# Optimization experiments

Measured on AMD Instinct MI355X. Metric: run time of the kernel, lower is better.

The kernel has to match this reference:

```python
import jax, jax.numpy as jnp
import numpy as np

B, T, D_IN, H, D_MU, K = 512, 256, 64, 256, 32, 8
EPS = 1e-09
ALPHA = 1.0


def setup_inputs() -> dict:
    key = jax.random.key(0)
    ks = jax.random.split(key, 32)
    def n(k, shape, s=0.05):
        return (jax.random.normal(k, shape) * s).astype(jnp.float32)
    X = jax.random.normal(ks[0], (B, T, D_IN), dtype=jnp.float32)
    missing_mask = (jax.random.uniform(ks[1], (B, T, D_IN)) < 0.8).astype(jnp.float32)
    noise = jax.random.normal(ks[2], (B, D_MU), dtype=jnp.float32)
    return dict(
        X=X, missing_mask=missing_mask, noise=noise,
        W_imp=n(ks[3], (D_IN, D_IN)),
        enc_Wih=n(ks[4], (4 * H, D_IN)), enc_bih=n(ks[5], (4 * H,)),
        enc_Whh=n(ks[6], (4 * H, H)), enc_bhh=n(ks[7], (4 * H,)),
        enc_Wch=n(ks[8], (3 * H, H)), enc_bch=n(ks[9], (3 * H,)),
        dec_Wih=n(ks[10], (4 * H, D_IN)), dec_bih=n(ks[11], (4 * H,)),
        dec_Whh=n(ks[12], (4 * H, H)), dec_bhh=n(ks[13], (4 * H,)),
        dec_Wch=n(ks[14], (3 * H, H)), dec_bch=n(ks[15], (3 * H,)),
        ae_enc_W=n(ks[16], (H, H)), ae_enc_b=n(ks[17], (H,)),
        ae_dec_W=n(ks[18], (H, D_MU)), ae_dec_b=n(ks[19], (H,)),
        mu_W=n(ks[20], (D_MU, H)), mu_b=n(ks[21], (D_MU,)),
        std_W=n(ks[22], (D_MU, H)), std_b=n(ks[23], (D_MU,)),
        out_W=n(ks[24], (D_IN, H)), out_b=n(ks[25], (D_IN,)),
        mu_c_u=n(ks[26], (K, D_MU)), var_c_u=n(ks[27], (K, D_MU)),
        phi_c_u=n(ks[28], (K,)),
    )


def _peephole_scan(xs, h0, c0, Wih, bih, Whh, bhh, Wch, bch):
    # xs: [T, B, D]; peephole LSTM with 3H-wide cell->gate weights (i, f, o),
    # gate layout of the 4H preactivation is (i, f, g, o) with g getting no peephole.
    Hd = h0.shape[1]
    def step(carry, x):
        h, c = carry
        wx = x @ Wih.T + bih          # [B, 4H]
        wh = h @ Whh.T + bhh          # [B, 4H]
        wc = c @ Wch.T + bch          # [B, 3H]
        wc_full = jnp.concatenate(
            [wc[:, :2 * Hd], jnp.zeros_like(h), wc[:, 2 * Hd:]], axis=1)
        s = wx + wh + wc_full
        i = jax.nn.sigmoid(s[:, :Hd])
        f = jax.nn.sigmoid(s[:, Hd:2 * Hd])
        g = jnp.tanh(s[:, 2 * Hd:3 * Hd])
        o = jax.nn.sigmoid(s[:, 3 * Hd:])
        c_new = f * c + i * g
        h_new = o * jnp.tanh(c_new)
        return (h_new, c_new), h_new
    (h, c), hs = jax.lax.scan(step, (h0, c0), xs)
    return h, c, hs


def reference(X, missing_mask, noise, W_imp,
              enc_Wih, enc_bih, enc_Whh, enc_bhh, enc_Wch, enc_bch,
              dec_Wih, dec_bih, dec_Whh, dec_bhh, dec_Wch, dec_bch,
              ae_enc_W, ae_enc_b, ae_dec_W, ae_dec_b,
              mu_W, mu_b, std_W, std_b, out_W, out_b,
              mu_c_u, var_c_u, phi_c_u):
    b, t, d_in = X.shape
    # --- implicit imputation (faithful to original, incl. (1 - X) factor) ---
    imputation = jnp.einsum('btd,ed->bte', X, W_imp)
    X_imputed = X * missing_mask + imputation * (1.0 - X)
    # --- encode: peephole LSTM over time ---
    h0 = jnp.zeros((b, H), dtype=X.dtype)
    c0 = jnp.zeros((b, H), dtype=X.dtype)
    xs = jnp.swapaxes(X_imputed, 0, 1)  # [T, B, D]
    _, c_T, _ = _peephole_scan(xs, h0, c0, enc_Wih, enc_bih, enc_Whh, enc_bhh, enc_Wch, enc_bch)
    cell_coll = jax.nn.softplus(c_T @ ae_enc_W.T + ae_enc_b)
    mu_tilde = cell_coll @ mu_W.T + mu_b
    stddev_tilde = cell_coll @ std_W.T + std_b
    z = mu_tilde + jnp.exp(0.5 * stddev_tilde) * noise
    # --- decode: zero inputs, h0 = softplus(linear(z)) ---
    h0d = jax.nn.softplus(z @ ae_dec_W.T + ae_dec_b)
    c0d = jnp.zeros_like(h0d)
    zeros_in = jnp.zeros((t, b, d_in), dtype=z.dtype)
    _, _, hs = _peephole_scan(zeros_in, h0d, c0d, dec_Wih, dec_bih, dec_Whh, dec_bhh, dec_Wch, dec_bch)
    hidden_coll = jnp.swapaxes(hs, 0, 1)  # [B, T, H]
    X_rec = jnp.einsum('bth,dh->btd', hidden_coll, out_W) + out_b
    # --- GMM layer ---
    mu_c = mu_c_u                              # [K, D_MU]
    var_c = jax.nn.softplus(var_c_u)           # [K, D_MU]
    phi_c = jax.nn.softmax(phi_c_u)            # [K]
    # --- reconstruction loss (masked MSE) ---
    mask_sum = jnp.sum(missing_mask)
    mse = jnp.sum(missing_mask * jnp.square(X_rec - X)) / (mask_sum + 1e-12)
    recon_loss = mse * t * d_in / mask_sum
    # --- latent loss ---
    var_tilde = jnp.exp(stddev_tilde)          # [B, D_MU]
    stddev_c = jnp.log(var_c + EPS)            # [K, D_MU]
    log_2pi = jnp.log(jnp.array(2.0 * np.pi, dtype=X.dtype))
    log_phi_c = jnp.log(phi_c + EPS)           # [K]
    diff = z[:, None, :] - mu_c[None, :, :]    # [B, K, D]
    log_pdf_z = -0.5 * (stddev_c[None] + log_2pi + jnp.square(diff) / var_c[None])
    log_p = log_phi_c[None, :] + log_pdf_z.sum(axis=2)          # [B, K]
    log_gamma_c = log_p - jax.nn.logsumexp(log_p, axis=1, keepdims=True)
    gamma_c = jnp.exp(log_gamma_c)
    term1 = jnp.log(var_c + EPS)[None]                           # [1, K, D]
    term2 = var_tilde[:, None, :] / (var_c[None] + EPS)          # [B, K, D]
    term3 = jnp.square(mu_tilde[:, None, :] - mu_c[None]) / (var_c[None] + EPS)
    latent1 = 0.5 * jnp.sum(gamma_c * jnp.sum(term1 + term2 + term3, axis=2), axis=1)
    latent2 = -jnp.sum(gamma_c * (log_phi_c[None, :] - log_gamma_c), axis=1)
    latent3 = -0.5 * jnp.sum(1.0 + stddev_tilde, axis=1)
    latent_loss = latent1.mean() + latent2.mean() + latent3.mean()
    loss = recon_loss + ALPHA * latent_loss
    return loss, z
```

## Files before the change

kernel.cpp:

```cpp
#include <hip/hip_runtime.h>
#include <math.h>

#define NBLK 256
#define NTHR 512

constexpr float EPSF = 1e-9f;
constexpr float LOG2PIF = 1.8378770664093453f;

constexpr size_t OFF_CNT  = 0;
constexpr size_t OFF_GEN  = 32;
constexpr size_t OFF_PART = 128;
constexpr size_t WENC = 4096;
constexpr size_t BENC = WENC + (size_t)1024 * 576;
constexpr size_t WDEC = BENC + 1024;
constexpr size_t BDEC = WDEC + (size_t)1024 * 512;
constexpr size_t HBUF = BDEC + 1024;
constexpr size_t CBUF = HBUF + (size_t)2 * 512 * 256;
constexpr size_t XIMP = CBUF + (size_t)2 * 512 * 256;
constexpr size_t WS_NEED = XIMP + (size_t)2 * 512 * 64;

constexpr size_t SZ = (size_t)512 * 256;

__device__ __forceinline__ float sigm_(float x) { return 1.f / (1.f + expf(-x)); }
__device__ __forceinline__ float softplus_(float x) { return x > 20.f ? x : log1pf(expf(x)); }

__device__ __forceinline__ void gbar(float* ws) {
  __syncthreads();
  if (threadIdx.x == 0) {
    __threadfence();
    unsigned* cnt = (unsigned*)(ws + OFF_CNT);
    unsigned* gen = (unsigned*)(ws + OFF_GEN);
    unsigned g = __hip_atomic_load(gen, __ATOMIC_RELAXED, __HIP_MEMORY_SCOPE_AGENT);
    unsigned a = __hip_atomic_fetch_add(cnt, 1u, __ATOMIC_ACQ_REL, __HIP_MEMORY_SCOPE_AGENT);
    if (a == NBLK - 1) {
      __hip_atomic_store(cnt, 0u, __ATOMIC_RELAXED, __HIP_MEMORY_SCOPE_AGENT);
      __hip_atomic_store(gen, g + 1u, __ATOMIC_RELEASE, __HIP_MEMORY_SCOPE_AGENT);
    } else {
      while (__hip_atomic_load(gen, __ATOMIC_RELAXED, __HIP_MEMORY_SCOPE_AGENT) == g) {
        __builtin_amdgcn_s_sleep(2);
      }
    }
    __threadfence();
  }
  __syncthreads();
}

__global__ void vader_init(
    const float* __restrict__ eWih, const float* __restrict__ ebih,
    const float* __restrict__ eWhh, const float* __restrict__ ebhh,
    const float* __restrict__ eWch, const float* __restrict__ ebch,
    const float* __restrict__ dbih, const float* __restrict__ dWhh,
    const float* __restrict__ dbhh, const float* __restrict__ dWch,
    const float* __restrict__ dbch, float* __restrict__ ws) {
  const int i0 = blockIdx.x * blockDim.x + threadIdx.x;
  const int stride = gridDim.x * blockDim.x;
  for (int i = i0; i < 4096; i += stride) ws[i] = 0.f;
  for (int i = i0; i < 512 * 256; i += stride) {
    ws[HBUF + i] = 0.f;
    ws[CBUF + i] = 0.f;
  }
  for (int i = i0; i < 1024 * 576; i += stride) {
    int n = i / 576, k = i - n * 576;
    float v;
    if (k < 64)       v = eWih[n * 64 + k];
    else if (k < 320) v = eWhh[n * 256 + (k - 64)];
    else {
      int j = k - 320;
      if (n < 512)      v = eWch[n * 256 + j];
      else if (n < 768) v = 0.f;
      else              v = eWch[(n - 256) * 256 + j];
    }
    ws[WENC + i] = v;
  }
  for (int i = i0; i < 1024 * 512; i += stride) {
    int n = i >> 9, k = i & 511;
    float v;
    if (k < 256) v = dWhh[n * 256 + k];
    else {
      int j = k - 256;
      if (n < 512)      v = dWch[n * 256 + j];
      else if (n < 768) v = 0.f;
      else              v = dWch[(n - 256) * 256 + j];
    }
    ws[WDEC + i] = v;
  }
  for (int i = i0; i < 1024; i += stride) {
    float bce = (i < 512) ? ebch[i] : ((i < 768) ? 0.f : ebch[i - 256]);
    ws[BENC + i] = ebih[i] + ebhh[i] + bce;
    float bcd = (i < 512) ? dbch[i] : ((i < 768) ? 0.f : dbch[i - 256]);
    ws[BDEC + i] = dbih[i] + dbhh[i] + bcd;
  }
}

__global__ __launch_bounds__(NTHR, 2) void vader_main(
    const float* __restrict__ X, const float* __restrict__ MM, const float* __restrict__ NZ,
    const float* __restrict__ Wimp,
    const float* __restrict__ aeW, const float* __restrict__ aeb,
    const float* __restrict__ adW, const float* __restrict__ adb,
    const float* __restrict__ muW, const float* __restrict__ mub,
    const float* __restrict__ stW, const float* __restrict__ stb,
    const float* __restrict__ oW, const float* __restrict__ ob,
    const float* __restrict__ mcu, const float* __restrict__ vcu, const float* __restrict__ pcu,
    float* __restrict__ ws, float* __restrict__ out) {
  const int bid = blockIdx.x, tid = threadIdx.x;
  const int mi = bid & 7, hi = bid >> 3;
  const int m_base = mi << 6;
  const int hbase = hi << 3;
  const int b0 = bid << 1;

  __shared__ __align__(16) float In_s[2][64][68];
  __shared__ __align__(16) float W_s[32][576];
  __shared__ __align__(16) char u1_raw[17408];
  __shared__ __align__(16) char u2_raw[8192];
  __shared__ float C_s[64][9];
  __shared__ float Xrow_s[2][64], Mrow_s[2][64];
  __shared__ float lat_s[2][3];
  __shared__ float tot_s[5];

  float (*WimpT_s)[68] = (float(*)[68])u1_raw;
  float (*Wo_s)[260]   = (float(*)[260])u1_raw;
  float (*Xm_s)[12]    = (float(*)[12])(u1_raw + 8320);
  float (*Mm_s)[12]    = (float(*)[12])(u1_raw + 8320 + 3072);
  float* GateS         = (float*)u2_raw;
  float (*Hrow_s)[256] = (float(*)[256])u2_raw;
  float (*cc_s)[256]   = (float(*)[256])(u2_raw + 2048);
  float (*mu_s)[32]    = (float(*)[32])(u2_raw + 4096);
  float (*std_s)[32]   = (float(*)[32])(u2_raw + 4352);
  float (*z_s)[32]     = (float(*)[32])(u2_raw + 4608);
  float* red_s         = (float*)u2_raw;

  float* hbuf = ws + HBUF;
  float* cbuf = ws + CBUF;
  float* ximp = ws + XIMP;
  float* part = ws + OFF_PART;

  const int mA = tid & 31, nP = tid >> 5;
  const int n0 = nP << 1, n1 = n0 + 1;
  const int N0 = ((n0 >> 3) << 8) + hbase + (n0 & 7);
  const int N1 = ((n1 >> 3) << 8) + hbase + (n1 & 7);
  const int st_r = tid >> 3, st_c4 = tid & 7;
  const int mX = tid & 63, dX = tid >> 6;
  const int um = tid >> 3, uh = tid & 7;
  const bool mse_blk = (hi < 8);

  float ssq_acc = 0.f, msum_acc = 0.f;

  auto stage_ld = [&](const float* src, int srd, int koff, float4& v0, float4& v1) {
    const float* bp = src + (size_t)(m_base + st_r) * srd + koff + (st_c4 << 2);
    v0 = *(const float4*)bp;
    v1 = *(const float4*)(bp + 32);
  };
  auto stage_wr = [&](int buf, float4 v0, float4 v1) {
    float* q = &In_s[buf][st_r][st_c4 << 2];
    *(float4*)q = v0;
    *(float4*)(q + 32) = v1;
  };
  auto chunk_src_enc = [&](int ch, int t, int pp, const float*& src, int& srd, int& koff) {
    if (ch == 0)      { src = ximp + (size_t)(t & 1) * (512 * 64); srd = 64;  koff = 0; }
    else if (ch < 5)  { src = hbuf + (size_t)pp * SZ; srd = 256; koff = (ch - 1) << 6; }
    else              { src = cbuf + (size_t)pp * SZ; srd = 256; koff = (ch - 5) << 6; }
  };
  auto chunk_src_dec = [&](int ch, int pp, const float*& src, int& srd, int& koff) {
    if (ch < 4) { src = hbuf + (size_t)pp * SZ; srd = 256; koff = ch << 6; }
    else        { src = cbuf + (size_t)pp * SZ; srd = 256; koff = (ch - 4) << 6; }
  };
  auto gates_chunk = [&](int buf, int ch, float& a00, float& a01, float& a10, float& a11) {
    const float* w0p = &W_s[n0][ch << 6];
    const float* w1p = &W_s[n1][ch << 6];
#pragma unroll
    for (int k4 = 0; k4 < 16; ++k4) {
      float4 w0 = *(const float4*)(w0p + (k4 << 2));
      float4 w1 = *(const float4*)(w1p + (k4 << 2));
      float4 a0 = *(const float4*)&In_s[buf][mA][k4 << 2];
      float4 a1 = *(const float4*)&In_s[buf][mA + 32][k4 << 2];
      a00 = fmaf(a0.x, w0.x, a00); a00 = fmaf(a0.y, w0.y, a00);
      a00 = fmaf(a0.z, w0.z, a00); a00 = fmaf(a0.w, w0.w, a00);
      a01 = fmaf(a0.x, w1.x, a01); a01 = fmaf(a0.y, w1.y, a01);
      a01 = fmaf(a0.z, w1.z, a01); a01 = fmaf(a0.w, w1.w, a01);
      a10 = fmaf(a1.x, w0.x, a10); a10 = fmaf(a1.y, w0.y, a10);
      a10 = fmaf(a1.z, w0.z, a10); a10 = fmaf(a1.w, w0.w, a10);
      a11 = fmaf(a1.x, w1.x, a11); a11 = fmaf(a1.y, w1.y, a11);
      a11 = fmaf(a1.z, w1.z, a11); a11 = fmaf(a1.w, w1.w, a11);
    }
  };
  auto xrec_chunk = [&](int buf, int ch, float& ax) {
    const float* wp = &Wo_s[dX][ch << 6];
#pragma unroll
    for (int k4 = 0; k4 < 16; ++k4) {
      float4 w = *(const float4*)(wp + (k4 << 2));
      float4 av = *(const float4*)&In_s[buf][mX][k4 << 2];
      ax = fmaf(av.x, w.x, ax);
      ax = fmaf(av.y, w.y, ax);
      ax = fmaf(av.z, w.z, ax);
      ax = fmaf(av.w, w.w, ax);
    }
  };
  auto do_update = [&](float a00, float a01, float a10, float a11, float* hbo, float* cbo) {
    GateS[((n0 >> 3) << 9) + (mA << 3) + (n0 & 7)] = a00;
    GateS[((n0 >> 3) << 9) + ((mA + 32) << 3) + (n0 & 7)] = a10;
    GateS[((n1 >> 3) << 9) + (mA << 3) + (n1 & 7)] = a01;
    GateS[((n1 >> 3) << 9) + ((mA + 32) << 3) + (n1 & 7)] = a11;
    __syncthreads();
    float iv = sigm_(GateS[(0 << 9) + (um << 3) + uh]);
    float fv = sigm_(GateS[(1 << 9) + (um << 3) + uh]);
    float gv = tanhf(GateS[(2 << 9) + (um << 3) + uh]);
    float ov = sigm_(GateS[(3 << 9) + (um << 3) + uh]);
    float cold = C_s[um][uh];
    float cn = fmaf(fv, cold, iv * gv);
    float hn = ov * tanhf(cn);
    C_s[um][uh] = cn;
    size_t off = (size_t)(m_base + um) * 256 + hbase + uh;
    hbo[off] = hn;
    cbo[off] = cn;
  };
  auto produce_ximp = [&](int tn) {
    if (tid < 128) {
      int r = tid >> 6, d = tid & 63;
      Xrow_s[r][d] = X[((size_t)(b0 + r) * 256 + tn) * 64 + d];
    } else if (tid < 256) {
      int r = (tid >> 6) & 1, d = tid & 63;
      Mrow_s[r][d] = MM[((size_t)(b0 + r) * 256 + tn) * 64 + d];
    }
    __syncthreads();
    if (tid < 128) {
      int r = tid >> 6, d = tid & 63;
      float s = 0.f;
#pragma unroll 8
      for (int e = 0; e < 64; ++e) s = fmaf(Xrow_s[r][e], WimpT_s[e][d], s);
      float x = Xrow_s[r][d];
      ximp[(size_t)(tn & 1) * (512 * 64) + (size_t)(b0 + r) * 64 + d] =
          fmaf(x, Mrow_s[r][d], s * (1.f - x));
    }
  };

  {
    int n = tid >> 4, c16 = tid & 15;
    const float* wsrc = ws + WENC + (size_t)(((n >> 3) << 8) + hbase + (n & 7)) * 576;
#pragma unroll
    for (int j = 0; j < 9; ++j) {
      int c4 = c16 * 9 + j;
      *(float4*)&W_s[n][c4 << 2] = *(const float4*)&wsrc[c4 << 2];
    }
    for (int i = tid; i < 4096; i += NTHR) {
      int d = i >> 6, e = i & 63;
      WimpT_s[e][d] = Wimp[i];
    }
    for (int i = tid; i < 576; i += NTHR) ((float*)C_s)[i] = 0.f;
  }
  float bia0 = ws[BENC + N0], bia1 = ws[BENC + N1];
  produce_ximp(0);
  gbar(ws);

  int p = 0;
  for (int t = 0; t < 256; ++t) {
    float a00 = bia0, a01 = bia1, a10 = bia0, a11 = bia1;
    float4 r0, r1;
    const float* src; int srd, koff;
    chunk_src_enc(0, t, p, src, srd, koff);
    stage_ld(src, srd, koff, r0, r1);
    stage_wr(0, r0, r1);
    __syncthreads();
    for (int ch = 0; ch < 9; ++ch) {
      if (ch < 8) { chunk_src_enc(ch + 1, t, p, src, srd, koff); stage_ld(src, srd, koff, r0, r1); }
      gates_chunk(ch & 1, ch, a00, a01, a10, a11);
      if (ch < 8) stage_wr((ch + 1) & 1, r0, r1);
      __syncthreads();
    }
    do_update(a00, a01, a10, a11, hbuf + (size_t)(p ^ 1) * SZ, cbuf + (size_t)(p ^ 1) * SZ);
    if (t < 255) produce_ximp(t + 1);
    gbar(ws);
    p ^= 1;
  }

  {
    int rr = tid >> 8, j = tid & 255;
    Hrow_s[rr][j] = cbuf[(size_t)(b0 + rr) * 256 + j];
  }
  __syncthreads();
  {
    int rr = tid >> 8, u = tid & 255;
    float a = aeb[u];
    const float4* wr = (const float4*)(aeW + (size_t)u * 256);
#pragma unroll 4
    for (int j4 = 0; j4 < 64; ++j4) {
      float4 w = wr[j4];
      a = fmaf(Hrow_s[rr][(j4 << 2) + 0], w.x, a);
      a = fmaf(Hrow_s[rr][(j4 << 2) + 1], w.y, a);
      a = fmaf(Hrow_s[rr][(j4 << 2) + 2], w.z, a);
      a = fmaf(Hrow_s[rr][(j4 << 2) + 3], w.w, a);
    }
    cc_s[rr][u] = softplus_(a);
  }
  __syncthreads();
  if (tid < 128) {
    int rr = tid >> 6, sel = (tid >> 5) & 1, q = tid & 31;
    const float* Wm = sel ? stW : muW;
    float a = sel ? stb[q] : mub[q];
    const float4* wr = (const float4*)(Wm + (size_t)q * 256);
#pragma unroll 4
    for (int j4 = 0; j4 < 64; ++j4) {
      float4 w = wr[j4];
      a = fmaf(cc_s[rr][(j4 << 2) + 0], w.x, a);
      a = fmaf(cc_s[rr][(j4 << 2) + 1], w.y, a);
      a = fmaf(cc_s[rr][(j4 << 2) + 2], w.z, a);
      a = fmaf(cc_s[rr][(j4 << 2) + 3], w.w, a);
    }
    if (sel) std_s[rr][q] = a; else mu_s[rr][q] = a;
  }
  __syncthreads();
  if (tid < 64) {
    int rr = tid >> 5, q = tid & 31;
    float zv = fmaf(expf(0.5f * std_s[rr][q]), NZ[(size_t)(b0 + rr) * 32 + q], mu_s[rr][q]);
    z_s[rr][q] = zv;
    out[1 + (size_t)(b0 + rr) * 32 + q] = zv;
  }
  __syncthreads();
  {
    int rr = tid >> 8, u = tid & 255;
    float a = adb[u];
#pragma unroll
    for (int q = 0; q < 32; ++q) a = fmaf(z_s[rr][q], adW[(size_t)u * 32 + q], a);
    hbuf[(size_t)(b0 + rr) * 256 + u] = softplus_(a);
    cbuf[(size_t)(b0 + rr) * 256 + u] = 0.f;
  }
  if (tid < 128) {
    int wv = tid >> 6, ln = tid & 63;
    if (ln < 32) {
      float zd = z_s[wv][ln], mud = mu_s[wv][ln], sdd = std_s[wv][ln];
      float vt = expf(sdd);
      float l3p = -0.5f * (1.f + sdd);
      float lp[8], tk[8];
#pragma unroll
      for (int k = 0; k < 8; ++k) {
        float vc = softplus_(vcu[(k << 5) + ln]);
        float lvc = logf(vc + EPSF);
        float mc = mcu[(k << 5) + ln];
        float dz = zd - mc;
        float a_d = lvc + LOG2PIF + dz * dz / vc;
        float ive = 1.f / (vc + EPSF);
        float dm = mud - mc;
        float t_d = lvc + fmaf(vt, ive, dm * dm * ive);
#pragma unroll
        for (int off = 16; off > 0; off >>= 1) {
          a_d += __shfl_xor(a_d, off, 64);
          t_d += __shfl_xor(t_d, off, 64);
        }
        lp[k] = -0.5f * a_d;
        tk[k] = t_d;
      }
#pragma unroll
      for (int off = 16; off > 0; off >>= 1) l3p += __shfl_xor(l3p, off, 64);
      float phv[8], mx = -1e30f;
#pragma unroll
      for (int k = 0; k < 8; ++k) { phv[k] = pcu[k]; mx = fmaxf(mx, phv[k]); }
      float se = 0.f;
#pragma unroll
      for (int k = 0; k < 8; ++k) se += expf(phv[k] - mx);
      float lphi[8], lpf[8], mx2 = -1e30f;
#pragma unroll
      for (int k = 0; k < 8; ++k) {
        lphi[k] = logf(expf(phv[k] - mx) / se + EPSF);
        lpf[k] = lphi[k] + lp[k];
        mx2 = fmaxf(mx2, lpf[k]);
      }
      float s2 = 0.f;
#pragma unroll
      for (int k = 0; k < 8; ++k) s2 += expf(lpf[k] - mx2);
      float lse = mx2 + logf(s2);
      float l1 = 0.f, l2 = 0.f;
#pragma unroll
      for (int k = 0; k < 8; ++k) {
        float lg = lpf[k] - lse;
        float gm = expf(lg);
        l1 = fmaf(gm, tk[k], l1);
        l2 = fmaf(gm, lphi[k] - lg, l2);
      }
      if (ln == 0) {
        lat_s[wv][0] = 0.5f * l1;
        lat_s[wv][1] = -l2;
        lat_s[wv][2] = l3p;
      }
    }
  }
  __syncthreads();

  {
    int n = tid >> 4, c16 = tid & 15;
    const float* wsrc = ws + WDEC + (size_t)(((n >> 3) << 8) + hbase + (n & 7)) * 512;
#pragma unroll
    for (int j = 0; j < 8; ++j) {
      int c4 = (c16 << 3) + j;
      *(float4*)&W_s[n][c4 << 2] = *(const float4*)&wsrc[c4 << 2];
    }
    if (mse_blk) {
      int r = tid >> 6, c4 = tid & 63;
      *(float4*)&Wo_s[r][c4 << 2] = *(const float4*)&oW[(size_t)((hi << 3) + r) * 256 + (c4 << 2)];
    }
    for (int i = tid; i < 576; i += NTHR) ((float*)C_s)[i] = 0.f;
  }
  float bia0d = ws[BDEC + N0], bia1d = ws[BDEC + N1];
  float obv = mse_blk ? ob[(hi << 3) + dX] : 0.f;
  gbar(ws);

  for (int t = 0; t <= 256; ++t) {
    const bool dg = (t < 256);
    const bool dm = mse_blk && (t >= 1);
    const int NC = dg ? 8 : 4;
    float a00 = bia0d, a01 = bia1d, a10 = bia0d, a11 = bia1d;
    float ax = 0.f;
    float4 r0, r1;
    const float* src; int srd, koff;
    chunk_src_dec(0, p, src, srd, koff);
    stage_ld(src, srd, koff, r0, r1);
    stage_wr(0, r0, r1);
    if (dm) {
      if (tid < 128) {
        int r2 = tid >> 1, hf = tid & 1;
        *(float4*)&Xm_s[r2][hf << 2] =
            *(const float4*)&X[((size_t)(m_base + r2) * 256 + (t - 1)) * 64 + (hi << 3) + (hf << 2)];
      } else if (tid < 256) {
        int r2 = (tid - 128) >> 1, hf = tid & 1;
        *(float4*)&Mm_s[r2][hf << 2] =
            *(const float4*)&MM[((size_t)(m_base + r2) * 256 + (t - 1)) * 64 + (hi << 3) + (hf << 2)];
      }
    }
    __syncthreads();
    for (int ch = 0; ch < NC; ++ch) {
      if (ch + 1 < NC) { chunk_src_dec(ch + 1, p, src, srd, koff); stage_ld(src, srd, koff, r0, r1); }
      if (dg) gates_chunk(ch & 1, ch, a00, a01, a10, a11);
      if (dm && ch < 4) xrec_chunk(ch & 1, ch, ax);
      if (ch + 1 < NC) stage_wr((ch + 1) & 1, r0, r1);
      __syncthreads();
    }
    if (dm) {
      float xr = ax + obv;
      float df = xr - Xm_s[mX][dX];
      float mv = Mm_s[mX][dX];
      ssq_acc = fmaf(mv, df * df, ssq_acc);
      msum_acc += mv;
    }
    if (dg) {
      do_update(a00, a01, a10, a11, hbuf + (size_t)(p ^ 1) * SZ, cbuf + (size_t)(p ^ 1) * SZ);
      gbar(ws);
      p ^= 1;
    }
  }

  red_s[tid] = ssq_acc;
  __syncthreads();
  for (int s = 256; s > 0; s >>= 1) { if (tid < s) red_s[tid] += red_s[tid + s]; __syncthreads(); }
  if (tid == 0) part[(bid << 3) + 0] = red_s[0];
  __syncthreads();
  red_s[tid] = msum_acc;
  __syncthreads();
  for (int s = 256; s > 0; s >>= 1) { if (tid < s) red_s[tid] += red_s[tid + s]; __syncthreads(); }
  if (tid == 0) {
    part[(bid << 3) + 1] = red_s[0];
    part[(bid << 3) + 2] = lat_s[0][0] + lat_s[1][0];
    part[(bid << 3) + 3] = lat_s[0][1] + lat_s[1][1];
    part[(bid << 3) + 4] = lat_s[0][2] + lat_s[1][2];
  }
  gbar(ws);

  if (bid == 0) {
    for (int c = 0; c < 5; ++c) {
      red_s[tid] = (tid < 256) ? part[(tid << 3) + c] : 0.f;
      __syncthreads();
      for (int s = 256; s > 0; s >>= 1) { if (tid < s) red_s[tid] += red_s[tid + s]; __syncthreads(); }
      if (tid == 0) tot_s[c] = red_s[0];
      __syncthreads();
    }
    if (tid == 0) {
      float ssq = tot_s[0], msum = tot_s[1];
      float mse = ssq / (msum + 1e-12f);
      float recon = mse * 16384.f / msum;
      float latent = (tot_s[2] + tot_s[3] + tot_s[4]) / 512.f;
      out[0] = recon + latent;
    }
  }
}

extern "C" void kernel_launch(void* const* d_in, const int* in_sizes, int n_in,
                              void* d_out, int out_size, void* d_ws, size_t ws_size,
                              hipStream_t stream) {
  (void)in_sizes; (void)out_size;
  if (n_in < 29) return;
  if (ws_size < WS_NEED * sizeof(float)) return;
  const float* X    = (const float*)d_in[0];
  const float* MM   = (const float*)d_in[1];
  const float* NZ   = (const float*)d_in[2];
  const float* Wimp = (const float*)d_in[3];
  const float* eWih = (const float*)d_in[4];
  const float* ebih = (const float*)d_in[5];
  const float* eWhh = (const float*)d_in[6];
  const float* ebhh = (const float*)d_in[7];
  const float* eWch = (const float*)d_in[8];
  const float* ebch = (const float*)d_in[9];
  const float* dbih = (const float*)d_in[11];
  const float* dWhh = (const float*)d_in[12];
  const float* dbhh = (const float*)d_in[13];
  const float* dWch = (const float*)d_in[14];
  const float* dbch = (const float*)d_in[15];
  const float* aeW  = (const float*)d_in[16];
  const float* aeb  = (const float*)d_in[17];
  const float* adW  = (const float*)d_in[18];
  const float* adb  = (const float*)d_in[19];
  const float* muW  = (const float*)d_in[20];
  const float* mub  = (const float*)d_in[21];
  const float* stW  = (const float*)d_in[22];
  const float* stb  = (const float*)d_in[23];
  const float* oW   = (const float*)d_in[24];
  const float* ob   = (const float*)d_in[25];
  const float* mcu  = (const float*)d_in[26];
  const float* vcu  = (const float*)d_in[27];
  const float* pcu  = (const float*)d_in[28];
  float* ws = (float*)d_ws;

  vader_init<<<512, 256, 0, stream>>>(eWih, ebih, eWhh, ebhh, eWch, ebch,
                                      dbih, dWhh, dbhh, dWch, dbch, ws);
  vader_main<<<NBLK, NTHR, 0, stream>>>(X, MM, NZ, Wimp, aeW, aeb, adW, adb,
                                        muW, mub, stW, stb, oW, ob, mcu, vcu, pcu,
                                        ws, (float*)d_out);
}
```

Before: 16.46 ms.

## Replace grid-wide step barriers with per-batch-group barriers of 32 blocks

Each block works on a fixed slice of 64 batch rows (mi), and the recurrent h/c state only needs to be exchanged among the 32 blocks that share that batch slice. The per-timestep grid barrier over all 256 blocks becomes 8 independent group barriers, each with its own counter and generation word. Only the final reduction keeps a full barrier. The post-encoder row assignment b0 is remapped so each block reads only rows its own group produced. This cuts atomic contention and barrier latency on the recurrent critical path, but correctness now depends on the dependency analysis being exact.

```diff
diff --git a/kernel.cpp b/kernel.cpp
--- a/kernel.cpp
+++ b/kernel.cpp
@@ -7,9 +7,11 @@
 constexpr float EPSF = 1e-9f;
 constexpr float LOG2PIF = 1.8378770664093453f;
 
-constexpr size_t OFF_CNT  = 0;
-constexpr size_t OFF_GEN  = 32;
-constexpr size_t OFF_PART = 128;
+constexpr size_t OFF_GCNT = 0;
+constexpr size_t OFF_GGEN = 256;
+constexpr size_t OFF_FCNT = 512;
+constexpr size_t OFF_FGEN = 544;
+constexpr size_t OFF_PART = 1024;
 constexpr size_t WENC = 4096;
 constexpr size_t BENC = WENC + (size_t)1024 * 576;
 constexpr size_t WDEC = BENC + 1024;
@@ -24,12 +26,33 @@
 __device__ __forceinline__ float sigm_(float x) { return 1.f / (1.f + expf(-x)); }
 __device__ __forceinline__ float softplus_(float x) { return x > 20.f ? x : log1pf(expf(x)); }
 
-__device__ __forceinline__ void gbar(float* ws) {
+__device__ __forceinline__ void gbar_g(float* ws, int mi) {
   __syncthreads();
   if (threadIdx.x == 0) {
     __threadfence();
-    unsigned* cnt = (unsigned*)(ws + OFF_CNT);
-    unsigned* gen = (unsigned*)(ws + OFF_GEN);
+    unsigned* cnt = (unsigned*)(ws + OFF_GCNT + ((size_t)mi << 5));
+    unsigned* gen = (unsigned*)(ws + OFF_GGEN + ((size_t)mi << 5));
+    unsigned g = __hip_atomic_load(gen, __ATOMIC_RELAXED, __HIP_MEMORY_SCOPE_AGENT);
+    unsigned a = __hip_atomic_fetch_add(cnt, 1u, __ATOMIC_ACQ_REL, __HIP_MEMORY_SCOPE_AGENT);
+    if (a == 31u) {
+      __hip_atomic_store(cnt, 0u, __ATOMIC_RELAXED, __HIP_MEMORY_SCOPE_AGENT);
+      __hip_atomic_store(gen, g + 1u, __ATOMIC_RELEASE, __HIP_MEMORY_SCOPE_AGENT);
+    } else {
+      while (__hip_atomic_load(gen, __ATOMIC_RELAXED, __HIP_MEMORY_SCOPE_AGENT) == g) {
+        __builtin_amdgcn_s_sleep(2);
+      }
+    }
+    __threadfence();
+  }
+  __syncthreads();
+}
+
+__device__ __forceinline__ void gbar_full(float* ws) {
+  __syncthreads();
+  if (threadIdx.x == 0) {
+    __threadfence();
+    unsigned* cnt = (unsigned*)(ws + OFF_FCNT);
+    unsigned* gen = (unsigned*)(ws + OFF_FGEN);
     unsigned g = __hip_atomic_load(gen, __ATOMIC_RELAXED, __HIP_MEMORY_SCOPE_AGENT);
     unsigned a = __hip_atomic_fetch_add(cnt, 1u, __ATOMIC_ACQ_REL, __HIP_MEMORY_SCOPE_AGENT);
     if (a == NBLK - 1) {
@@ -106,7 +129,7 @@
   const int mi = bid & 7, hi = bid >> 3;
   const int m_base = mi << 6;
   const int hbase = hi << 3;
-  const int b0 = bid << 1;
+  const int b0 = m_base + (hi << 1);
 
   __shared__ __align__(16) float In_s[2][64][68];
   __shared__ __align__(16) float W_s[32][576];
@@ -249,7 +272,7 @@
   }
   float bia0 = ws[BENC + N0], bia1 = ws[BENC + N1];
   produce_ximp(0);
-  gbar(ws);
+  gbar_g(ws, mi);
 
   int p = 0;
   for (int t = 0; t < 256; ++t) {
@@ -268,7 +291,7 @@
     }
     do_update(a00, a01, a10, a11, hbuf + (size_t)(p ^ 1) * SZ, cbuf + (size_t)(p ^ 1) * SZ);
     if (t < 255) produce_ximp(t + 1);
-    gbar(ws);
+    gbar_g(ws, mi);
     p ^= 1;
   }
 
@@ -400,7 +423,7 @@
   }
   float bia0d = ws[BDEC + N0], bia1d = ws[BDEC + N1];
   float obv = mse_blk ? ob[(hi << 3) + dX] : 0.f;
-  gbar(ws);
+  gbar_g(ws, mi);
 
   for (int t = 0; t <= 256; ++t) {
     const bool dg = (t < 256);
@@ -441,7 +464,7 @@
     }
     if (dg) {
       do_update(a00, a01, a10, a11, hbuf + (size_t)(p ^ 1) * SZ, cbuf + (size_t)(p ^ 1) * SZ);
-      gbar(ws);
+      gbar_g(ws, mi);
       p ^= 1;
     }
   }
@@ -460,7 +483,7 @@
     part[(bid << 3) + 3] = lat_s[0][1] + lat_s[1][1];
     part[(bid << 3) + 4] = lat_s[0][2] + lat_s[1][2];
   }
-  gbar(ws);
+  gbar_full(ws);
 
   if (bid == 0) {
     for (int c = 0; c < 5; ++c) {
```

Measured after the change: 15.76 ms. -4.3%, faster.
